# Performance work log

Hardware: AMD Instinct MI355X
Metric: run time of the kernel (lower is better)

## Reference

```python
import jax, jax.numpy as jnp
import numpy as np
from jax import lax

L = 64          # filter_length
C = 64          # n_channels
B = 64          # batch
T = 4096        # time steps per call


def _sliding_max(a, k):
    # a: [B, C, T + k - 1] -> [B, C, T], windowed max, stride 1, VALID
    return lax.reduce_window(a, -jnp.inf, lax.max, (1, 1, k), (1, 1, 1), 'VALID')


def setup_inputs() -> dict:
    key = jax.random.key(0)
    x = jax.random.normal(key, (B, C, T), dtype=jnp.float32)
    # State buffers as lazily allocated by the module on first forward:
    prev_input = jnp.full((B, C, L - 1), -jnp.inf, dtype=jnp.float32)
    prev_max_out = jnp.full((B, C, L - 1), jnp.inf, dtype=jnp.float32)
    return {'x': x, 'prev_input': prev_input, 'prev_max_out': prev_max_out}


def reference(x, prev_input, prev_max_out):
    # max-pool over [prev_input, x] with kernel L, stride 1 (causal streaming max)
    max_input = jnp.concatenate([prev_input, x], axis=-1)        # [B, C, T+L-1]
    max_out = _sliding_max(max_input, L)                         # [B, C, T]
    # min-pool over [prev_max_out, max_out] via negated max-pool
    min_input = jnp.concatenate([prev_max_out, max_out], axis=-1)  # [B, C, T+L-1]
    out = -_sliding_max(-min_input, L)                           # [B, C, T]
    return out
```

## Files before the change

kernel.cpp:

```cpp
#include <hip/hip_runtime.h>
#include <math.h>


#define TT    4096
#define PADN  63
#define XPMAX 4158

struct __attribute__((packed, aligned(4))) f4u { float x, y, z, w; };

template<int CTRL>
__device__ __forceinline__ float dpp_self(float v) {
  return __int_as_float(__builtin_amdgcn_update_dpp(
      __float_as_int(v), __float_as_int(v), CTRL, 0xF, 0xF, false));
}
template<int CTRL>
__device__ __forceinline__ float dpp_old(float oldv, float v) {
  return __int_as_float(__builtin_amdgcn_update_dpp(
      __float_as_int(oldv), __float_as_int(v), CTRL, 0xF, 0xF, false));
}

template<bool IS_MAX>
__device__ __forceinline__ void chunk_windows(float4 a0, float4 a1, float r[4]) {
  const float ID = IS_MAX ? -INFINITY : INFINITY;
#define OPF(x, y) (IS_MAX ? fmaxf((x), (y)) : fminf((x), (y)))
  float s3 = a0.w;
  float s2 = OPF(a0.z, s3);
  float s1 = OPF(a0.y, s2);
  float s0 = OPF(a0.x, s1);
  float t = s0;
  t = OPF(t, dpp_self<0x101>(t));
  t = OPF(t, dpp_self<0x102>(t));
  t = OPF(t, dpp_self<0x104>(t));
  t = OPF(t, dpp_self<0x108>(t));
  float E = dpp_old<0x101>(ID, t);

  float p0 = a1.x;
  float p1 = OPF(p0, a1.y);
  float p2 = OPF(p1, a1.z);
  float p3 = OPF(p2, a1.w);
  float u = p3;
  u = OPF(u, dpp_self<0x111>(u));
  u = OPF(u, dpp_self<0x112>(u));
  u = OPF(u, dpp_self<0x114>(u));
  u = OPF(u, dpp_self<0x118>(u));
  float Ep = dpp_old<0x111>(ID, u);

  r[0] = OPF(OPF(s0, E), Ep);
  r[1] = OPF(OPF(s1, E), OPF(Ep, p0));
  r[2] = OPF(OPF(s2, E), OPF(Ep, p1));
  r[3] = OPF(OPF(s3, E), OPF(Ep, p2));
#undef OPF
}

__device__ __forceinline__ float4 load_slab(int t0, int l16,
                                            const float* __restrict__ xrow,
                                            const float* __restrict__ pirow) {
  if (t0 >= PADN && t0 <= TT - 1) {
    f4u v = *reinterpret_cast<const f4u*>(xrow + t0 - PADN + 4 * l16);
    return make_float4(v.x, v.y, v.z, v.w);
  }
  float e[4];
  #pragma unroll
  for (int k = 0; k < 4; ++k) {
    const int q = t0 + 4 * l16 + k;
    float v;
    if (q < 0)           v = -INFINITY;
    else if (q < PADN)   v = pirow[q];
    else if (q <= XPMAX) v = xrow[q - PADN];
    else                 v = -INFINITY;
    e[k] = v;
  }
  return make_float4(e[0], e[1], e[2], e[3]);
}

__global__ __launch_bounds__(256)
void mmh_kernel(const float* __restrict__ x,
                const float* __restrict__ prev_input,
                const float* __restrict__ prev_max_out,
                float* __restrict__ out)
{
    const int tid  = threadIdx.x;
    const int lane = tid & 63;
    const int wv   = tid >> 6;
    const int l16  = lane & 15;
    const int rrow = lane >> 4;

    const int row   = blockIdx.x >> 2;
    const int wbase = ((blockIdx.x & 3) * 4 + wv) * 256;
    const int qA    = wbase + 64 * rrow;

    const float* xrow  = x            + (size_t)row * TT;
    const float* pirow = prev_input   + (size_t)row * PADN;
    const float* pmrow = prev_max_out + (size_t)row * PADN;
    float*       orow  = out          + (size_t)row * TT;

    const float4 X0 = load_slab(qA - 63, l16, xrow, pirow);
    const float4 X1 = load_slab(qA + 1,  l16, xrow, pirow);
    const float4 X2 = load_slab(qA + 65, l16, xrow, pirow);

    float mA[4], mB[4];
    chunk_windows<true>(X0, X1, mA);
    chunk_windows<true>(X1, X2, mB);

    if (qA == 0) {
        #pragma unroll
        for (int k = 0; k < 4; ++k) {
            const int p = 4 * l16 + k;
            if (p < PADN) mA[k] = pmrow[p];
        }
    }

    const float4 a0 = make_float4(mA[0], mA[1], mA[2], mA[3]);
    const float4 a1 = make_float4(mB[0], mB[1], mB[2], mB[3]);
    float r[4];
    chunk_windows<false>(a0, a1, r);

    *reinterpret_cast<float4*>(orow + qA + 4 * l16) =
        make_float4(r[0], r[1], r[2], r[3]);
}

extern "C" void kernel_launch(void* const* d_in, const int* in_sizes, int n_in,
                              void* d_out, int out_size, void* d_ws, size_t ws_size,
                              hipStream_t stream) {
    const float* x            = (const float*)d_in[0];
    const float* prev_input   = (const float*)d_in[1];
    const float* prev_max_out = (const float*)d_in[2];
    float*       out          = (float*)d_out;

    mmh_kernel<<<64 * 64 * 4, 256, 0, stream>>>(x, prev_input, prev_max_out, out);
}
```

Measured before the change: 126.9 us.

## Process 512-sample segments per 16-lane group to reuse loaded slabs

Each 16-lane group now computes eight consecutive 64-sample output chunks instead of one. It loads ten overlapping slabs once and reuses them for nine max-window stages and eight min-window stages. This removes the roughly threefold redundant loading and first-stage max computation of the one-chunk-per-group layout. In exchange it needs more registers per thread and launches fewer, longer-running blocks.

Result: faster. 117.4 us (-7.5%).

```diff
diff --git a/kernel.cpp b/kernel.cpp
--- a/kernel.cpp
+++ b/kernel.cpp
@@ -5,6 +5,10 @@
 #define TT    4096
 #define PADN  63
 #define XPMAX 4158
+#define SEG   512
+#define NSL   10
+#define NM    9
+#define NCH   8
 
 struct __attribute__((packed, aligned(4))) f4u { float x, y, z, w; };
 
@@ -80,43 +84,43 @@
                 float* __restrict__ out)
 {
     const int tid  = threadIdx.x;
-    const int lane = tid & 63;
-    const int wv   = tid >> 6;
-    const int l16  = lane & 15;
-    const int rrow = lane >> 4;
+    const int l16  = tid & 15;
+    const int rid  = blockIdx.x * 16 + (tid >> 4);
+    const int trow = rid >> 3;
+    const int S    = (rid & 7) * SEG;
 
-    const int row   = blockIdx.x >> 2;
-    const int wbase = ((blockIdx.x & 3) * 4 + wv) * 256;
-    const int qA    = wbase + 64 * rrow;
+    const float* xrow  = x            + (size_t)trow * TT;
+    const float* pirow = prev_input   + (size_t)trow * PADN;
+    const float* pmrow = prev_max_out + (size_t)trow * PADN;
+    float*       orow  = out          + (size_t)trow * TT;
 
-    const float* xrow  = x            + (size_t)row * TT;
-    const float* pirow = prev_input   + (size_t)row * PADN;
-    const float* pmrow = prev_max_out + (size_t)row * PADN;
-    float*       orow  = out          + (size_t)row * TT;
+    float4 L[NSL];
+    #pragma unroll
+    for (int j = 0; j < NSL; ++j)
+        L[j] = load_slab(S - 63 + 64 * j, l16, xrow, pirow);
 
-    const float4 X0 = load_slab(qA - 63, l16, xrow, pirow);
-    const float4 X1 = load_slab(qA + 1,  l16, xrow, pirow);
-    const float4 X2 = load_slab(qA + 65, l16, xrow, pirow);
+    float M[NM][4];
+    #pragma unroll
+    for (int j = 0; j < NM; ++j)
+        chunk_windows<true>(L[j], L[j + 1], M[j]);
 
-    float mA[4], mB[4];
-    chunk_windows<true>(X0, X1, mA);
-    chunk_windows<true>(X1, X2, mB);
-
-    if (qA == 0) {
+    if (S == 0) {
         #pragma unroll
         for (int k = 0; k < 4; ++k) {
             const int p = 4 * l16 + k;
-            if (p < PADN) mA[k] = pmrow[p];
+            if (p < PADN) M[0][k] = pmrow[p];
         }
     }
 
-    const float4 a0 = make_float4(mA[0], mA[1], mA[2], mA[3]);
-    const float4 a1 = make_float4(mB[0], mB[1], mB[2], mB[3]);
-    float r[4];
-    chunk_windows<false>(a0, a1, r);
-
-    *reinterpret_cast<float4*>(orow + qA + 4 * l16) =
-        make_float4(r[0], r[1], r[2], r[3]);
+    #pragma unroll
+    for (int j = 0; j < NCH; ++j) {
+        const float4 a0 = make_float4(M[j][0], M[j][1], M[j][2], M[j][3]);
+        const float4 a1 = make_float4(M[j + 1][0], M[j + 1][1], M[j + 1][2], M[j + 1][3]);
+        float r[4];
+        chunk_windows<false>(a0, a1, r);
+        *reinterpret_cast<float4*>(orow + S + 64 * j + 4 * l16) =
+            make_float4(r[0], r[1], r[2], r[3]);
+    }
 }
 
 extern "C" void kernel_launch(void* const* d_in, const int* in_sizes, int n_in,
@@ -127,5 +131,5 @@
     const float* prev_max_out = (const float*)d_in[2];
     float*       out          = (float*)d_out;
 
-    mmh_kernel<<<64 * 64 * 4, 256, 0, stream>>>(x, prev_input, prev_max_out, out);
+    mmh_kernel<<<2048, 256, 0, stream>>>(x, prev_input, prev_max_out, out);
 }
```
